# Kernel optimization log

Hardware: AMD Instinct MI355X
Metric: run time of the kernel (lower is better)

Reference implementation:

```python
import jax, jax.numpy as jnp
import numpy as np

COMMITMENT_COST = 0.25


def setup_inputs() -> dict:
    key = jax.random.key(0)
    k1, k2 = jax.random.split(key)
    B, K, D = 1048576, 16, 64
    z = jax.random.normal(k1, (B, D), dtype=jnp.float32)
    # nn.Embedding init: uniform(-1/K, 1/K)
    embedding = jax.random.uniform(k2, (K, D), dtype=jnp.float32,
                                   minval=-1.0 / K, maxval=1.0 / K)
    return {"z": z, "embedding": embedding}


def reference(z, embedding):
    # squared L2 distances: ||z||^2 + ||e||^2 - 2 z e^T  -> [B, K]
    distances = (jnp.sum(z * z, axis=1, keepdims=True)
                 + jnp.sum(embedding * embedding, axis=1)
                 - 2.0 * jnp.matmul(z, embedding.T))
    encoding_indices = jnp.argmin(distances, axis=1)           # [B]
    quantized = embedding[encoding_indices]                    # [B, D]

    commitment_loss = jnp.mean((z - jax.lax.stop_gradient(quantized)) ** 2)
    embedding_loss = jnp.mean((jax.lax.stop_gradient(z) - quantized) ** 2)
    vq_loss = embedding_loss + COMMITMENT_COST * commitment_loss

    # straight-through estimator
    quantized = z + jax.lax.stop_gradient(quantized - z)
    return quantized, encoding_indices, vq_loss
```

## Files before the change

kernel.cpp:

```cpp
#include <hip/hip_runtime.h>

#define B_ROWS 1048576
#define K_CODES 16
#define D_DIM 64

constexpr int BLOCK = 256;
constexpr int GRID  = 2048;

typedef float f32x4 __attribute__((ext_vector_type(4)));

__device__ __forceinline__ float xor1_dpp(float x) {
    return __builtin_bit_cast(float,
        __builtin_amdgcn_update_dpp(0, __builtin_bit_cast(int, x), 0xB1, 0xF, 0xF, true));
}
__device__ __forceinline__ float xor2_dpp(float x) {
    return __builtin_bit_cast(float,
        __builtin_amdgcn_update_dpp(0, __builtin_bit_cast(int, x), 0x4E, 0xF, 0xF, true));
}
__device__ __forceinline__ float xor7_dpp(float x) {
    return __builtin_bit_cast(float,
        __builtin_amdgcn_update_dpp(0, __builtin_bit_cast(int, x), 0x141, 0xF, 0xF, true));
}
__device__ __forceinline__ float xor15_dpp(float x) {
    return __builtin_bit_cast(float,
        __builtin_amdgcn_update_dpp(0, __builtin_bit_cast(int, x), 0x140, 0xF, 0xF, true));
}

__global__ __launch_bounds__(BLOCK)
void vq_main(const float* __restrict__ z,
             const float* __restrict__ emb,
             float* __restrict__ out_q,
             float* __restrict__ out_idx,
             float* __restrict__ partials)
{
    __shared__ __align__(16) float s_emb[K_CODES * D_DIM];
    __shared__ float s_se[K_CODES];
    __shared__ float s_w[BLOCK / 64];

    const int t = threadIdx.x;

    ((float4*)s_emb)[t] = ((const float4*)emb)[t];
    __syncthreads();

    if (t < K_CODES) {
        float s = 0.f;
        #pragma unroll
        for (int c = 0; c < D_DIM; ++c) {
            float e = s_emb[t * D_DIM + c];
            s = fmaf(e, e, s);
        }
        s_se[t] = s;
    }
    __syncthreads();

    const int j = t & 15;
    const int sj = ((j & 1) ? 8 : 0) ^ ((j & 2) ? 4 : 0)
                 ^ ((j & 4) ? 14 : 0) ^ ((j & 8) ? 3 : 0);

    float4 ereg[16];
    #pragma unroll
    for (int r = 0; r < 16; ++r)
        ereg[r] = *(const float4*)&s_emb[((r ^ j) * D_DIM) + sj * 4];
    const float se_j = s_se[j];

    float lossacc = 0.f;

    const int gid    = (blockIdx.x * BLOCK + t) >> 4;
    const int stride = (GRID * BLOCK) >> 4;

    int row = gid;
    f32x4 zv = __builtin_nontemporal_load((const f32x4*)&z[(size_t)row * D_DIM + sj * 4]);

    while (row < B_ROWS) {
        const int nrow = row + stride;
        f32x4 zn = zv;
        if (nrow < B_ROWS)
            zn = __builtin_nontemporal_load((const f32x4*)&z[(size_t)nrow * D_DIM + sj * 4]);

        float p[16];
        #pragma unroll
        for (int r = 0; r < 16; ++r) {
            float4 e = ereg[r];
            p[r] = fmaf(zv.w, e.w, fmaf(zv.z, e.z, fmaf(zv.y, e.y, zv.x * e.x)));
        }

        float szp = fmaf(zv.w, zv.w, fmaf(zv.z, zv.z, fmaf(zv.y, zv.y, zv.x * zv.x)));
        szp += xor1_dpp(szp);
        szp += xor2_dpp(szp);
        szp += xor7_dpp(szp);
        szp += xor15_dpp(szp);

        #pragma unroll
        for (int r = 0; r < 8; ++r)  p[r] += xor15_dpp(p[15 - r]);
        #pragma unroll
        for (int r = 0; r < 4; ++r)  p[r] += xor7_dpp(p[7 - r]);
        p[0] += xor2_dpp(p[2]);
        p[1] += xor2_dpp(p[3]);
        p[0] += xor1_dpp(p[1]);
        const float dot = p[0];

        const float d = (szp + se_j) - 2.0f * dot;

        float vmin = d;
        vmin = fminf(vmin, xor1_dpp(vmin));
        vmin = fminf(vmin, xor2_dpp(vmin));
        vmin = fminf(vmin, xor7_dpp(vmin));
        vmin = fminf(vmin, xor15_dpp(vmin));
        unsigned long long bal = __ballot(d == vmin);
        unsigned int mask = (unsigned int)((bal >> (t & 48)) & 0xFFFFull);
        int kmin = __ffs(mask) - 1;

        const float4 qv = *(const float4*)&s_emb[kmin * D_DIM + sj * 4];

        float dx = zv.x - qv.x; lossacc = fmaf(dx, dx, lossacc);
        dx = zv.y - qv.y;       lossacc = fmaf(dx, dx, lossacc);
        dx = zv.z - qv.z;       lossacc = fmaf(dx, dx, lossacc);
        dx = zv.w - qv.w;       lossacc = fmaf(dx, dx, lossacc);

        f32x4 qn = { qv.x, qv.y, qv.z, qv.w };
        __builtin_nontemporal_store(qn, (f32x4*)&out_q[(size_t)row * D_DIM + sj * 4]);
        if (j == 0) out_idx[row] = (float)kmin;

        zv  = zn;
        row = nrow;
    }

    lossacc += __shfl_xor(lossacc, 32, 64);
    lossacc += __shfl_xor(lossacc, 16, 64);
    lossacc += __shfl_xor(lossacc, 8, 64);
    lossacc += __shfl_xor(lossacc, 4, 64);
    lossacc += __shfl_xor(lossacc, 2, 64);
    lossacc += __shfl_xor(lossacc, 1, 64);
    if ((t & 63) == 0) s_w[t >> 6] = lossacc;
    __syncthreads();
    if (t == 0) partials[blockIdx.x] = (s_w[0] + s_w[1]) + (s_w[2] + s_w[3]);
}

__global__ void vq_finalize(const float* __restrict__ partials, int n,
                            float* __restrict__ out_loss)
{
    __shared__ float sw[4];
    float s = 0.f;
    for (int i = threadIdx.x; i < n; i += 256) s += partials[i];
    s += __shfl_xor(s, 32, 64);
    s += __shfl_xor(s, 16, 64);
    s += __shfl_xor(s, 8, 64);
    s += __shfl_xor(s, 4, 64);
    s += __shfl_xor(s, 2, 64);
    s += __shfl_xor(s, 1, 64);
    if ((threadIdx.x & 63) == 0) sw[threadIdx.x >> 6] = s;
    __syncthreads();
    if (threadIdx.x == 0) {
        float tot = (sw[0] + sw[1]) + (sw[2] + sw[3]);
        *out_loss = tot * (1.25f / (float)(B_ROWS * (size_t)D_DIM));
    }
}

extern "C" void kernel_launch(void* const* d_in, const int* in_sizes, int n_in,
                              void* d_out, int out_size, void* d_ws, size_t ws_size,
                              hipStream_t stream)
{
    const float* z   = (const float*)d_in[0];
    const float* emb = (const float*)d_in[1];
    float* out      = (float*)d_out;
    float* out_q    = out;
    float* out_idx  = out + (size_t)B_ROWS * D_DIM;
    float* out_loss = out_idx + B_ROWS;
    float* partials = (float*)d_ws;

    vq_main<<<GRID, BLOCK, 0, stream>>>(z, emb, out_q, out_idx, partials);
    vq_finalize<<<1, 256, 0, stream>>>(partials, GRID, out_loss);
}
```

Before: 107.7 us.

## Split VQ into index pass and separate quantized-output gather pass

```diff
diff --git a/kernel.cpp b/kernel.cpp
--- a/kernel.cpp
+++ b/kernel.cpp
@@ -27,11 +27,10 @@
 }
 
 __global__ __launch_bounds__(BLOCK)
-void vq_main(const float* __restrict__ z,
-             const float* __restrict__ emb,
-             float* __restrict__ out_q,
-             float* __restrict__ out_idx,
-             float* __restrict__ partials)
+void vq_pass1(const float* __restrict__ z,
+              const float* __restrict__ emb,
+              float* __restrict__ out_idx,
+              float* __restrict__ partials)
 {
     __shared__ __align__(16) float s_emb[K_CODES * D_DIM];
     __shared__ float s_se[K_CODES];
@@ -111,14 +110,11 @@
         int kmin = __ffs(mask) - 1;
 
         const float4 qv = *(const float4*)&s_emb[kmin * D_DIM + sj * 4];
-
         float dx = zv.x - qv.x; lossacc = fmaf(dx, dx, lossacc);
         dx = zv.y - qv.y;       lossacc = fmaf(dx, dx, lossacc);
         dx = zv.z - qv.z;       lossacc = fmaf(dx, dx, lossacc);
         dx = zv.w - qv.w;       lossacc = fmaf(dx, dx, lossacc);
 
-        f32x4 qn = { qv.x, qv.y, qv.z, qv.w };
-        __builtin_nontemporal_store(qn, (f32x4*)&out_q[(size_t)row * D_DIM + sj * 4]);
         if (j == 0) out_idx[row] = (float)kmin;
 
         zv  = zn;
@@ -136,23 +132,56 @@
     if (t == 0) partials[blockIdx.x] = (s_w[0] + s_w[1]) + (s_w[2] + s_w[3]);
 }
 
-__global__ void vq_finalize(const float* __restrict__ partials, int n,
-                            float* __restrict__ out_loss)
+__global__ __launch_bounds__(BLOCK)
+void vq_pass2(const float* __restrict__ emb,
+              const float* __restrict__ idxf,
+              float* __restrict__ out_q,
+              const float* __restrict__ partials,
+              float* __restrict__ out_loss)
 {
+    __shared__ __align__(16) float s_emb[K_CODES * D_DIM];
     __shared__ float sw[4];
-    float s = 0.f;
-    for (int i = threadIdx.x; i < n; i += 256) s += partials[i];
-    s += __shfl_xor(s, 32, 64);
-    s += __shfl_xor(s, 16, 64);
-    s += __shfl_xor(s, 8, 64);
-    s += __shfl_xor(s, 4, 64);
-    s += __shfl_xor(s, 2, 64);
-    s += __shfl_xor(s, 1, 64);
-    if ((threadIdx.x & 63) == 0) sw[threadIdx.x >> 6] = s;
-    __syncthreads();
-    if (threadIdx.x == 0) {
-        float tot = (sw[0] + sw[1]) + (sw[2] + sw[3]);
-        *out_loss = tot * (1.25f / (float)(B_ROWS * (size_t)D_DIM));
+
+    const int t = threadIdx.x;
+
+    ((float4*)s_emb)[t] = ((const float4*)emb)[t];
+    __syncthreads();
+
+    if (blockIdx.x == 0) {
+        float s = 0.f;
+        for (int i = t; i < GRID; i += 256) s += partials[i];
+        s += __shfl_xor(s, 32, 64);
+        s += __shfl_xor(s, 16, 64);
+        s += __shfl_xor(s, 8, 64);
+        s += __shfl_xor(s, 4, 64);
+        s += __shfl_xor(s, 2, 64);
+        s += __shfl_xor(s, 1, 64);
+        if ((t & 63) == 0) sw[t >> 6] = s;
+        __syncthreads();
+        if (t == 0) {
+            float tot = (sw[0] + sw[1]) + (sw[2] + sw[3]);
+            *out_loss = tot * (1.25f / (float)(B_ROWS * (size_t)D_DIM));
+        }
+    }
+
+    const int j = t & 15;
+    const int gid    = (blockIdx.x * BLOCK + t) >> 4;
+    const int stride = (GRID * BLOCK) >> 4;
+
+    int row = gid;
+    float kf = idxf[row];
+
+    while (row < B_ROWS) {
+        const int nrow = row + stride;
+        float kn = kf;
+        if (nrow < B_ROWS) kn = idxf[nrow];
+
+        const int k = (int)kf;
+        const f32x4 qv = *(const f32x4*)&s_emb[k * D_DIM + j * 4];
+        __builtin_nontemporal_store(qv, (f32x4*)&out_q[(size_t)row * D_DIM + j * 4]);
+
+        kf  = kn;
+        row = nrow;
     }
 }
 
@@ -168,6 +197,6 @@
     float* out_loss = out_idx + B_ROWS;
     float* partials = (float*)d_ws;
 
-    vq_main<<<GRID, BLOCK, 0, stream>>>(z, emb, out_q, out_idx, partials);
-    vq_finalize<<<1, 256, 0, stream>>>(partials, GRID, out_loss);
-}
+    vq_pass1<<<GRID, BLOCK, 0, stream>>>(z, emb, out_idx, partials);
+    vq_pass2<<<GRID, BLOCK, 0, stream>>>(emb, out_idx, out_q, partials, out_loss);
+}
```

New measurement: 116.2 us. 7.9% more time.
